# Kernel optimization log

Hardware: AMD Instinct MI355X
Metric: run time of the kernel (lower is better)

The kernel has to match this reference:

```python
import jax, jax.numpy as jnp
import numpy as np

IN_DIM = 256
OUT_DIM = 64   # per-head dim
NUM_HEADS = 8
B = 8
N = 1024


def setup_inputs() -> dict:
    key = jax.random.key(0)
    k_adj, k_h, kq, kk, kv, kbq, kbk, kbv = jax.random.split(key, 8)
    adj_matrix = jax.random.randint(k_adj, (N, N), 0, 2, dtype=jnp.int32)
    h = jax.random.normal(k_h, (B, N, IN_DIM), dtype=jnp.float32)
    s = 1.0 / np.sqrt(IN_DIM)
    Wq = jax.random.normal(kq, (IN_DIM, OUT_DIM * NUM_HEADS), dtype=jnp.float32) * s
    Wk = jax.random.normal(kk, (IN_DIM, OUT_DIM * NUM_HEADS), dtype=jnp.float32) * s
    Wv = jax.random.normal(kv, (IN_DIM, OUT_DIM * NUM_HEADS), dtype=jnp.float32) * s
    bq = jax.random.normal(kbq, (OUT_DIM * NUM_HEADS,), dtype=jnp.float32) * 0.01
    bk = jax.random.normal(kbk, (OUT_DIM * NUM_HEADS,), dtype=jnp.float32) * 0.01
    bv = jax.random.normal(kbv, (OUT_DIM * NUM_HEADS,), dtype=jnp.float32) * 0.01
    return {"adj_matrix": adj_matrix, "h": h, "Wq": Wq, "bq": bq,
            "Wk": Wk, "bk": bk, "Wv": Wv, "bv": bv}


def reference(adj_matrix, h, Wq, bq, Wk, bk, Wv, bv):
    B_, N_, _ = h.shape
    H, D = NUM_HEADS, OUT_DIM
    Qh = (h @ Wq + bq).reshape(B_, N_, H, D)
    Kh = (h @ Wk + bk).reshape(B_, N_, H, D)
    Vh = (h @ Wv + bv).reshape(B_, N_, H, D)
    scores = jnp.einsum('bnhd,bmhd->bhnm', Qh, Kh) / jnp.sqrt(jnp.float32(D))
    # adjacency mask broadcast over batch and heads (neigh_attention=True)
    scores = jnp.where(adj_matrix[None, None, :, :] == 0, -jnp.inf, scores)
    attn = jax.nn.softmax(scores, axis=-1)
    out = jnp.einsum('bhnm,bmhd->bnhd', attn, Vh)
    return out.reshape(B_, N_, H * D)
```

## Files before the change

### kernel.cpp

```cpp
#include <hip/hip_runtime.h>
#include <math.h>

#define IN_DIM 256
#define HD     512
#define NHEADS 8
#define DH     64
#define NSEQ   1024
#define BATCH  8

#define QSCALE 0.18033688011112042f

typedef unsigned short u16;
typedef unsigned int   u32;
typedef unsigned long long u64;
typedef short bf16x8 __attribute__((ext_vector_type(8)));
typedef float f32x4  __attribute__((ext_vector_type(4)));

#if __has_builtin(__builtin_amdgcn_exp2f)
#define EXP2(x) __builtin_amdgcn_exp2f(x)
#else
#define EXP2(x) __expf(0.69314718056f * (x))
#endif

static __device__ __forceinline__ u16 f2bf(float x) {
    u32 u = __builtin_bit_cast(u32, x);
    u += 0x7FFFu + ((u >> 16) & 1u);
    return (u16)(u >> 16);
}
static __device__ __forceinline__ float bf2f(u16 x) {
    return __builtin_bit_cast(float, ((u32)x) << 16);
}
static __device__ __forceinline__ u32 pk(u16 a, u16 b) {
    return (u32)a | ((u32)b << 16);
}
static __device__ __forceinline__ u32 cvtpk(float a, float b) {
    return pk(f2bf(a), f2bf(b));
}

__global__ __launch_bounds__(256)
void prep_kernel(const float* __restrict__ Wq, const float* __restrict__ Wk,
                 const float* __restrict__ Wv, const int* __restrict__ adj,
                 u16* __restrict__ Wt, u16* __restrict__ MaddT)
{
    __shared__ u32 shpool[64 * 65];
    const int bid = blockIdx.x, tid = threadIdx.x;

    if (bid < 96) {
        float* tile = (float*)shpool;
        const int wk = bid;
        const int k0 = (wk & 3) * 64, n0 = ((wk >> 2) & 7) * 64, wsel = wk >> 5;
        const float* W = (wsel == 0) ? Wq : (wsel == 1) ? Wk : Wv;
        u16* Out = Wt + (size_t)wsel * HD * IN_DIM;

        const int r = tid >> 2, c0 = (tid & 3) * 16;
#pragma unroll
        for (int j = 0; j < 16; j += 4) {
            float4 v = *(const float4*)(W + (size_t)(k0 + r) * HD + n0 + c0 + j);
            tile[r * 65 + c0 + j + 0] = v.x; tile[r * 65 + c0 + j + 1] = v.y;
            tile[r * 65 + c0 + j + 2] = v.z; tile[r * 65 + c0 + j + 3] = v.w;
        }
        __syncthreads();
        const int n = tid >> 2, ks = (tid & 3) * 16;
        u16 o[16];
#pragma unroll
        for (int j = 0; j < 16; ++j) o[j] = f2bf(tile[(ks + j) * 65 + n]);
        uint4 u0, u1;
        u0.x = pk(o[0], o[1]);   u0.y = pk(o[2], o[3]);
        u0.z = pk(o[4], o[5]);   u0.w = pk(o[6], o[7]);
        u1.x = pk(o[8], o[9]);   u1.y = pk(o[10], o[11]);
        u1.z = pk(o[12], o[13]); u1.w = pk(o[14], o[15]);
        u16* dst = Out + (size_t)(n0 + n) * IN_DIM + k0 + ks;
        *(uint4*)(dst) = u0;
        *(uint4*)(dst + 8) = u1;
    } else {
        int* tile = (int*)shpool;
        const int abid = bid - 96;
        const int tR = abid >> 4, tC = abid & 15;
        const int r = tid >> 2, cg = (tid & 3) * 16;
        const int* src = adj + (size_t)(tR * 64 + r) * NSEQ + tC * 64 + cg;
#pragma unroll
        for (int j = 0; j < 16; j += 4) {
            int4 a = *(const int4*)(src + j);
            tile[r * 65 + cg + j + 0] = a.x; tile[r * 65 + cg + j + 1] = a.y;
            tile[r * 65 + cg + j + 2] = a.z; tile[r * 65 + cg + j + 3] = a.w;
        }
        __syncthreads();
        const int kk = tid >> 2, qg = (tid & 3) * 16;
        u16 o[16];
#pragma unroll
        for (int j = 0; j < 16; ++j)
            o[j] = (tile[(qg + j) * 65 + kk] == 0) ? (u16)0xFF7F : (u16)0;
        uint4 u0, u1;
        u0.x = pk(o[0], o[1]);   u0.y = pk(o[2], o[3]);
        u0.z = pk(o[4], o[5]);   u0.w = pk(o[6], o[7]);
        u1.x = pk(o[8], o[9]);   u1.y = pk(o[10], o[11]);
        u1.z = pk(o[12], o[13]); u1.w = pk(o[14], o[15]);
        u16* dst = MaddT + (size_t)(tC * 64 + kk) * NSEQ + tR * 64 + qg;
        *(uint4*)(dst) = u0;
        *(uint4*)(dst + 8) = u1;
    }
}

__global__ __launch_bounds__(256, 2)
void qkv_gemm_kernel(const float* __restrict__ h, const u16* __restrict__ Wt,
                     const float* __restrict__ bq, const float* __restrict__ bk,
                     const float* __restrict__ bv,
                     u16* __restrict__ Qg, u16* __restrict__ Kg,
                     u16* __restrict__ Vtg)
{
    __shared__ u16 pool[128 * 64 + 3 * 64 * 64];
    u16* As = pool;
    u16* Bs = pool + 128 * 64;

    const int m0 = blockIdx.x * 128;
    const int hh = blockIdx.y;
    const int n0 = hh * 64;

    const int tid = threadIdx.x;
    const int w = tid >> 6, lane = tid & 63, l15 = lane & 15, quad = lane >> 4;
    const int sw = l15 & 7;

    f32x4 acc[3][2][4];
#pragma unroll
    for (int wh = 0; wh < 3; ++wh)
#pragma unroll
        for (int rs = 0; rs < 2; ++rs)
#pragma unroll
            for (int t = 0; t < 4; ++t) acc[wh][rs][t] = (f32x4){0.f, 0.f, 0.f, 0.f};

    const int arow = tid >> 1, acg = (tid & 1) * 4;
    const int brow = tid & 63, bgrp = tid >> 6;
    const float* srcA = h + (size_t)(m0 + arow) * IN_DIM;

    for (int kk = 0; kk < IN_DIM; kk += 64) {
        __syncthreads();
#pragma unroll
        for (int g = 0; g < 4; ++g) {
            const float* p = srcA + kk + (acg + g) * 8;
            float4 v0 = *(const float4*)(p);
            float4 v1 = *(const float4*)(p + 4);
            uint4 u;
            u.x = cvtpk(v0.x, v0.y); u.y = cvtpk(v0.z, v0.w);
            u.z = cvtpk(v1.x, v1.y); u.w = cvtpk(v1.z, v1.w);
            *(uint4*)&As[arow * 64 + (((acg + g) ^ (arow & 7)) * 8)] = u;
        }
#pragma unroll
        for (int i = 0; i < 6; ++i) {
            const int gc = bgrp * 6 + i;
            const int wh = gc >> 3, c8 = gc & 7;
            *(uint4*)&Bs[wh * 4096 + brow * 64 + ((c8 ^ (brow & 7)) * 8)] =
                *(const uint4*)(Wt + (size_t)wh * HD * IN_DIM +
                                (size_t)(n0 + brow) * IN_DIM + kk + c8 * 8);
        }
        __syncthreads();
        bf16x8 a[2][2];
#pragma unroll
        for (int rs = 0; rs < 2; ++rs) {
            const int ra = (w * 32 + rs * 16 + l15) * 64;
            a[rs][0] = *(const bf16x8*)&As[ra + ((quad ^ sw) * 8)];
            a[rs][1] = *(const bf16x8*)&As[ra + (((4 + quad) ^ sw) * 8)];
        }
#pragma unroll
        for (int t = 0; t < 4; ++t) {
            const int rb = (t * 16 + l15) * 64;
#pragma unroll
            for (int wh = 0; wh < 3; ++wh) {
                bf16x8 b0 = *(const bf16x8*)&Bs[wh * 4096 + rb + ((quad ^ sw) * 8)];
                bf16x8 b1 = *(const bf16x8*)&Bs[wh * 4096 + rb + (((4 + quad) ^ sw) * 8)];
#pragma unroll
                for (int rs = 0; rs < 2; ++rs) {
                    acc[wh][rs][t] = __builtin_amdgcn_mfma_f32_16x16x32_bf16(a[rs][0], b0, acc[wh][rs][t], 0, 0, 0);
                    acc[wh][rs][t] = __builtin_amdgcn_mfma_f32_16x16x32_bf16(a[rs][1], b1, acc[wh][rs][t], 0, 0, 0);
                }
            }
        }
    }

    for (int which = 0; which < 2; ++which) {
        u16* T = pool;
        const float* bias = (which == 0) ? bq : bk;
        u16* Out = (which == 0) ? Qg : Kg;
        const float scale = (which == 0) ? QSCALE : 1.0f;
        __syncthreads();
#pragma unroll
        for (int t = 0; t < 4; ++t) {
            const float bvv = bias[n0 + t * 16 + l15];
#pragma unroll
            for (int rs = 0; rs < 2; ++rs) {
                const int rowb = w * 32 + rs * 16 + quad * 4;
#pragma unroll
                for (int r = 0; r < 4; ++r)
                    T[(rowb + r) * 72 + t * 16 + l15] =
                        f2bf((acc[which][rs][t][r] + bvv) * scale);
            }
        }
        __syncthreads();
        const int row = tid >> 1, half = tid & 1;
        u16* dst = Out + (size_t)(m0 + row) * HD + n0 + half * 32;
        const u16* srcT = &T[row * 72 + half * 32];
#pragma unroll
        for (int i = 0; i < 4; ++i)
            *(uint4*)(dst + i * 8) = *(const uint4*)(srcT + i * 8);
    }

    {
        u16* T = pool;
        __syncthreads();
#pragma unroll
        for (int t = 0; t < 4; ++t) {
            const float bvv = bv[n0 + t * 16 + l15];
            const int trow = (t * 16 + l15) * 136;
#pragma unroll
            for (int rs = 0; rs < 2; ++rs) {
                const int base = w * 32 + rs * 16 + quad * 4;
                const int c64 = base >> 6;
                const int mloc = base & 63;
                const int cb = c64 * 64 + ((mloc & 15) * 4) + (mloc >> 4);
#pragma unroll
                for (int r = 0; r < 4; ++r)
                    T[trow + cb + 4 * r] = f2bf(acc[2][rs][t][r] + bvv);
            }
        }
        __syncthreads();
        const int b = m0 >> 10, nloc = m0 & 1023;
        const int d = tid >> 2, c = (tid & 3) * 32;
        u16* dst = Vtg + ((size_t)(b * NHEADS + hh) * DH + d) * NSEQ + nloc + c;
#pragma unroll
        for (int i = 0; i < 4; ++i)
            *(uint4*)(dst + i * 8) = *(uint4*)&T[d * 136 + c + i * 8];
    }
}

__global__ __launch_bounds__(512, 4)
void attn_kernel(const u16* __restrict__ MaddT, const u16* __restrict__ Qg,
                 const u16* __restrict__ Kg, const u16* __restrict__ Vtg,
                 float* __restrict__ out)
{
    __shared__ u16 Ks[2][64 * 64];
    __shared__ u16 Vs[2][64 * 64];
    __shared__ u16 Ps[128 * 64];

    const int tid = threadIdx.x;
    const int w = tid >> 6, lane = tid & 63, l15 = lane & 15, quad = lane >> 4;
    const int qt = blockIdx.x, bh = blockIdx.y;
    const int b = bh >> 3;
    const int n0 = qt * 128;
    const size_t rowbase = (size_t)b * NSEQ;
    const int colbase = (bh & 7) * DH;
    const int sw = l15 & 7;

    const u16* qrow = Qg + (rowbase + n0 + w * 16 + l15) * HD + colbase;
    const bf16x8 qa0 = *(const bf16x8*)(qrow + quad * 8);
    const bf16x8 qa1 = *(const bf16x8*)(qrow + 32 + quad * 8);

    const int srow = tid >> 3, c8w = tid & 7;
    const int swc = ((c8w ^ (srow & 7)) * 8);
    const u16* kgp = Kg + (rowbase + srow) * HD + colbase + c8w * 8;
    const u16* vgp = Vtg + ((size_t)bh * DH + srow) * NSEQ + c8w * 8;
    const u16* mgp = MaddT + (size_t)l15 * NSEQ + n0 + w * 16 + quad * 4;

    uint4 kG = *(const uint4*)kgp;
    uint4 vG = *(const uint4*)vgp;
    ushort4 mG[4];
#pragma unroll
    for (int t = 0; t < 4; ++t) mG[t] = *(const ushort4*)(mgp + (size_t)(t * 16) * NSEQ);

    *(uint4*)&Ks[0][srow * 64 + swc] = kG;
    *(uint4*)&Vs[0][srow * 64 + swc] = vG;
    __syncthreads();

    float lrow[4] = {0.f, 0.f, 0.f, 0.f};
    f32x4 O[4];
#pragma unroll
    for (int t = 0; t < 4; ++t) O[t] = (f32x4){0.f, 0.f, 0.f, 0.f};

    const int pwbase = (w * 16 + quad * 4) * 64;
    const int parow  = (w * 16 + l15) * 64;

    for (int ch = 0; ch < 16; ++ch) {
        const int cur = ch & 1;

        f32x4 s4[4];
#pragma unroll
        for (int t = 0; t < 4; ++t)
            s4[t] = (f32x4){bf2f(mG[t].x), bf2f(mG[t].y), bf2f(mG[t].z), bf2f(mG[t].w)};

        if (ch < 15) {
            kG = *(const uint4*)(kgp + (size_t)(ch + 1) * 64 * HD);
            vG = *(const uint4*)(vgp + (ch + 1) * 64);
#pragma unroll
            for (int t = 0; t < 4; ++t)
                mG[t] = *(const ushort4*)(mgp + ((size_t)(ch + 1) * 64 + t * 16) * NSEQ);
        }

#pragma unroll
        for (int t = 0; t < 4; ++t) {
            const int rb = (t * 16 + l15) * 64;
            bf16x8 kb0 = *(const bf16x8*)&Ks[cur][rb + ((quad ^ sw) * 8)];
            bf16x8 kb1 = *(const bf16x8*)&Ks[cur][rb + (((4 + quad) ^ sw) * 8)];
            s4[t] = __builtin_amdgcn_mfma_f32_16x16x32_bf16(qa0, kb0, s4[t], 0, 0, 0);
            s4[t] = __builtin_amdgcn_mfma_f32_16x16x32_bf16(qa1, kb1, s4[t], 0, 0, 0);
        }

        if (ch < 15) {
            *(uint4*)&Ks[1 - cur][srow * 64 + swc] = kG;
            *(uint4*)&Vs[1 - cur][srow * 64 + swc] = vG;
        }

#pragma unroll
        for (int r = 0; r < 4; ++r) {
            float p0 = EXP2(s4[0][r]);
            float p1 = EXP2(s4[1][r]);
            float p2 = EXP2(s4[2][r]);
            float p3 = EXP2(s4[3][r]);
            lrow[r] += (p0 + p1) + (p2 + p3);
            uint2 pw;
            pw.x = cvtpk(p0, p1);
            pw.y = cvtpk(p2, p3);
            const int q7 = (quad * 4 + r) & 7;
            *(uint2*)&Ps[pwbase + r * 64 + (((l15 >> 1) ^ q7) * 8) + (l15 & 1) * 4] = pw;
        }

        {
            bf16x8 pa0 = *(const bf16x8*)&Ps[parow + ((quad ^ sw) * 8)];
            bf16x8 pa1 = *(const bf16x8*)&Ps[parow + (((4 + quad) ^ sw) * 8)];
#pragma unroll
            for (int t = 0; t < 4; ++t) {
                const int rb = (t * 16 + l15) * 64;
                bf16x8 vb0 = *(const bf16x8*)&Vs[cur][rb + ((quad ^ sw) * 8)];
                bf16x8 vb1 = *(const bf16x8*)&Vs[cur][rb + (((4 + quad) ^ sw) * 8)];
                O[t] = __builtin_amdgcn_mfma_f32_16x16x32_bf16(pa0, vb0, O[t], 0, 0, 0);
                O[t] = __builtin_amdgcn_mfma_f32_16x16x32_bf16(pa1, vb1, O[t], 0, 0, 0);
            }
        }
        __syncthreads();
    }

#pragma unroll
    for (int d = 1; d < 16; d <<= 1)
#pragma unroll
        for (int r = 0; r < 4; ++r)
            lrow[r] += __shfl_xor(lrow[r], d, 64);

    float inv[4];
#pragma unroll
    for (int r = 0; r < 4; ++r) inv[r] = 1.0f / lrow[r];
#pragma unroll
    for (int t = 0; t < 4; ++t)
#pragma unroll
        for (int r = 0; r < 4; ++r)
            out[(rowbase + n0 + w * 16 + quad * 4 + r) * HD + colbase + t * 16 + l15] =
                O[t][r] * inv[r];
}

extern "C" void kernel_launch(void* const* d_in, const int* in_sizes, int n_in,
                              void* d_out, int out_size, void* d_ws, size_t ws_size,
                              hipStream_t stream) {
    const int*   adj = (const int*)d_in[0];
    const float* h   = (const float*)d_in[1];
    const float* Wq  = (const float*)d_in[2];
    const float* bq  = (const float*)d_in[3];
    const float* Wk  = (const float*)d_in[4];
    const float* bk  = (const float*)d_in[5];
    const float* Wv  = (const float*)d_in[6];
    const float* bv  = (const float*)d_in[7];
    float* outp = (float*)d_out;

    u16* Wt    = (u16*)d_ws;
    u16* Qg    = Wt + (size_t)3 * HD * IN_DIM;
    u16* Kg    = Qg + (size_t)BATCH * NSEQ * HD;
    u16* Vtg   = Kg + (size_t)BATCH * NSEQ * HD;
    u16* MaddT = Vtg + (size_t)BATCH * NSEQ * HD;

    prep_kernel<<<352, 256, 0, stream>>>(Wq, Wk, Wv, adj, Wt, MaddT);
    qkv_gemm_kernel<<<dim3(BATCH * NSEQ / 128, NHEADS), 256, 0, stream>>>(
        h, Wt, bq, bk, bv, Qg, Kg, Vtg);
    attn_kernel<<<dim3(NSEQ / 128, BATCH * NHEADS), 512, 0, stream>>>(
        MaddT, Qg, Kg, Vtg, outp);
}
```

Before: 142.8 us.

## Register-prefetch GEMM tiles and give each attention wave two row strips

The QKV GEMM now loads the next K-slice of h and W into registers while the current slice is computed, so global loads overlap the MFMAs. The attention kernel drops to 256 threads per block, and each wave handles 32 query rows instead of 16. This reuses every K/V LDS fragment across two MFMA row strips and halves the per-block cost of loading K and V tiles. The trade-off is higher register pressure and fewer waves to hide latency.

```diff
diff --git a/kernel.cpp b/kernel.cpp
--- a/kernel.cpp
+++ b/kernel.cpp
@@ -132,27 +132,50 @@
     const int brow = tid & 63, bgrp = tid >> 6;
     const float* srcA = h + (size_t)(m0 + arow) * IN_DIM;
 
+    float4 aF[8];
+    uint4  bF[6];
+#pragma unroll
+    for (int g = 0; g < 4; ++g) {
+        aF[2 * g]     = *(const float4*)(srcA + (acg + g) * 8);
+        aF[2 * g + 1] = *(const float4*)(srcA + (acg + g) * 8 + 4);
+    }
+#pragma unroll
+    for (int i = 0; i < 6; ++i) {
+        const int gc = bgrp * 6 + i, wh = gc >> 3, c8 = gc & 7;
+        bF[i] = *(const uint4*)(Wt + (size_t)wh * HD * IN_DIM +
+                                (size_t)(n0 + brow) * IN_DIM + c8 * 8);
+    }
+
     for (int kk = 0; kk < IN_DIM; kk += 64) {
         __syncthreads();
 #pragma unroll
         for (int g = 0; g < 4; ++g) {
-            const float* p = srcA + kk + (acg + g) * 8;
-            float4 v0 = *(const float4*)(p);
-            float4 v1 = *(const float4*)(p + 4);
             uint4 u;
-            u.x = cvtpk(v0.x, v0.y); u.y = cvtpk(v0.z, v0.w);
-            u.z = cvtpk(v1.x, v1.y); u.w = cvtpk(v1.z, v1.w);
+            u.x = cvtpk(aF[2 * g].x, aF[2 * g].y);
+            u.y = cvtpk(aF[2 * g].z, aF[2 * g].w);
+            u.z = cvtpk(aF[2 * g + 1].x, aF[2 * g + 1].y);
+            u.w = cvtpk(aF[2 * g + 1].z, aF[2 * g + 1].w);
             *(uint4*)&As[arow * 64 + (((acg + g) ^ (arow & 7)) * 8)] = u;
         }
 #pragma unroll
         for (int i = 0; i < 6; ++i) {
-            const int gc = bgrp * 6 + i;
-            const int wh = gc >> 3, c8 = gc & 7;
-            *(uint4*)&Bs[wh * 4096 + brow * 64 + ((c8 ^ (brow & 7)) * 8)] =
-                *(const uint4*)(Wt + (size_t)wh * HD * IN_DIM +
-                                (size_t)(n0 + brow) * IN_DIM + kk + c8 * 8);
-        }
-        __syncthreads();
+            const int gc = bgrp * 6 + i, wh = gc >> 3, c8 = gc & 7;
+            *(uint4*)&Bs[wh * 4096 + brow * 64 + ((c8 ^ (brow & 7)) * 8)] = bF[i];
+        }
+        __syncthreads();
+        if (kk + 64 < IN_DIM) {
+#pragma unroll
+            for (int g = 0; g < 4; ++g) {
+                aF[2 * g]     = *(const float4*)(srcA + kk + 64 + (acg + g) * 8);
+                aF[2 * g + 1] = *(const float4*)(srcA + kk + 64 + (acg + g) * 8 + 4);
+            }
+#pragma unroll
+            for (int i = 0; i < 6; ++i) {
+                const int gc = bgrp * 6 + i, wh = gc >> 3, c8 = gc & 7;
+                bF[i] = *(const uint4*)(Wt + (size_t)wh * HD * IN_DIM +
+                                        (size_t)(n0 + brow) * IN_DIM + kk + 64 + c8 * 8);
+            }
+        }
         bf16x8 a[2][2];
 #pragma unroll
         for (int rs = 0; rs < 2; ++rs) {
@@ -231,7 +254,7 @@
     }
 }
 
-__global__ __launch_bounds__(512, 4)
+__global__ __launch_bounds__(256, 3)
 void attn_kernel(const u16* __restrict__ MaddT, const u16* __restrict__ Qg,
                  const u16* __restrict__ Kg, const u16* __restrict__ Vtg,
                  float* __restrict__ out)
@@ -249,48 +272,63 @@
     const int colbase = (bh & 7) * DH;
     const int sw = l15 & 7;
 
-    const u16* qrow = Qg + (rowbase + n0 + w * 16 + l15) * HD + colbase;
-    const bf16x8 qa0 = *(const bf16x8*)(qrow + quad * 8);
-    const bf16x8 qa1 = *(const bf16x8*)(qrow + 32 + quad * 8);
-
-    const int srow = tid >> 3, c8w = tid & 7;
-    const int swc = ((c8w ^ (srow & 7)) * 8);
-    const u16* kgp = Kg + (rowbase + srow) * HD + colbase + c8w * 8;
-    const u16* vgp = Vtg + ((size_t)bh * DH + srow) * NSEQ + c8w * 8;
-    const u16* mgp = MaddT + (size_t)l15 * NSEQ + n0 + w * 16 + quad * 4;
-
-    uint4 kG = *(const uint4*)kgp;
-    uint4 vG = *(const uint4*)vgp;
-    ushort4 mG[4];
-#pragma unroll
-    for (int t = 0; t < 4; ++t) mG[t] = *(const ushort4*)(mgp + (size_t)(t * 16) * NSEQ);
-
-    *(uint4*)&Ks[0][srow * 64 + swc] = kG;
-    *(uint4*)&Vs[0][srow * 64 + swc] = vG;
+    bf16x8 qa[2][2];
+#pragma unroll
+    for (int rs = 0; rs < 2; ++rs) {
+        const u16* qrow = Qg + (rowbase + n0 + w * 32 + rs * 16 + l15) * HD + colbase;
+        qa[rs][0] = *(const bf16x8*)(qrow + quad * 8);
+        qa[rs][1] = *(const bf16x8*)(qrow + 32 + quad * 8);
+    }
+
+    const int srow = tid >> 2, cp = (tid & 3) * 2;
+    const int swc0 = ((cp ^ (srow & 7)) * 8), swc1 = (((cp + 1) ^ (srow & 7)) * 8);
+    const u16* kgp = Kg + (rowbase + srow) * HD + colbase + cp * 8;
+    const u16* vgp = Vtg + ((size_t)bh * DH + srow) * NSEQ + cp * 8;
+    const u16* mgp = MaddT + (size_t)l15 * NSEQ + n0 + w * 32 + quad * 4;
+
+    uint4 kG0 = *(const uint4*)kgp, kG1 = *(const uint4*)(kgp + 8);
+    uint4 vG0 = *(const uint4*)vgp, vG1 = *(const uint4*)(vgp + 8);
+    ushort4 mG[2][4];
+#pragma unroll
+    for (int rs = 0; rs < 2; ++rs)
+#pragma unroll
+        for (int t = 0; t < 4; ++t)
+            mG[rs][t] = *(const ushort4*)(mgp + (size_t)(t * 16) * NSEQ + rs * 16);
+
+    *(uint4*)&Ks[0][srow * 64 + swc0] = kG0;
+    *(uint4*)&Ks[0][srow * 64 + swc1] = kG1;
+    *(uint4*)&Vs[0][srow * 64 + swc0] = vG0;
+    *(uint4*)&Vs[0][srow * 64 + swc1] = vG1;
     __syncthreads();
 
-    float lrow[4] = {0.f, 0.f, 0.f, 0.f};
-    f32x4 O[4];
-#pragma unroll
-    for (int t = 0; t < 4; ++t) O[t] = (f32x4){0.f, 0.f, 0.f, 0.f};
-
-    const int pwbase = (w * 16 + quad * 4) * 64;
-    const int parow  = (w * 16 + l15) * 64;
+    float lrow[2][4] = {{0.f, 0.f, 0.f, 0.f}, {0.f, 0.f, 0.f, 0.f}};
+    f32x4 O[2][4];
+#pragma unroll
+    for (int rs = 0; rs < 2; ++rs)
+#pragma unroll
+        for (int t = 0; t < 4; ++t) O[rs][t] = (f32x4){0.f, 0.f, 0.f, 0.f};
 
     for (int ch = 0; ch < 16; ++ch) {
         const int cur = ch & 1;
 
-        f32x4 s4[4];
-#pragma unroll
-        for (int t = 0; t < 4; ++t)
-            s4[t] = (f32x4){bf2f(mG[t].x), bf2f(mG[t].y), bf2f(mG[t].z), bf2f(mG[t].w)};
+        f32x4 s4[2][4];
+#pragma unroll
+        for (int rs = 0; rs < 2; ++rs)
+#pragma unroll
+            for (int t = 0; t < 4; ++t)
+                s4[rs][t] = (f32x4){bf2f(mG[rs][t].x), bf2f(mG[rs][t].y),
+                                    bf2f(mG[rs][t].z), bf2f(mG[rs][t].w)};
 
         if (ch < 15) {
-            kG = *(const uint4*)(kgp + (size_t)(ch + 1) * 64 * HD);
-            vG = *(const uint4*)(vgp + (ch + 1) * 64);
-#pragma unroll
-            for (int t = 0; t < 4; ++t)
-                mG[t] = *(const ushort4*)(mgp + ((size_t)(ch + 1) * 64 + t * 16) * NSEQ);
+            kG0 = *(const uint4*)(kgp + (size_t)(ch + 1) * 64 * HD);
+            kG1 = *(const uint4*)(kgp + (size_t)(ch + 1) * 64 * HD + 8);
+            vG0 = *(const uint4*)(vgp + (ch + 1) * 64);
+            vG1 = *(const uint4*)(vgp + (ch + 1) * 64 + 8);
+#pragma unroll
+            for (int rs = 0; rs < 2; ++rs)
+#pragma unroll
+                for (int t = 0; t < 4; ++t)
+                    mG[rs][t] = *(const ushort4*)(mgp + ((size_t)(ch + 1) * 64 + t * 16) * NSEQ + rs * 16);
         }
 
 #pragma unroll
@@ -298,39 +336,55 @@
             const int rb = (t * 16 + l15) * 64;
             bf16x8 kb0 = *(const bf16x8*)&Ks[cur][rb + ((quad ^ sw) * 8)];
             bf16x8 kb1 = *(const bf16x8*)&Ks[cur][rb + (((4 + quad) ^ sw) * 8)];
-            s4[t] = __builtin_amdgcn_mfma_f32_16x16x32_bf16(qa0, kb0, s4[t], 0, 0, 0);
-            s4[t] = __builtin_amdgcn_mfma_f32_16x16x32_bf16(qa1, kb1, s4[t], 0, 0, 0);
+#pragma unroll
+            for (int rs = 0; rs < 2; ++rs) {
+                s4[rs][t] = __builtin_amdgcn_mfma_f32_16x16x32_bf16(qa[rs][0], kb0, s4[rs][t], 0, 0, 0);
+                s4[rs][t] = __builtin_amdgcn_mfma_f32_16x16x32_bf16(qa[rs][1], kb1, s4[rs][t], 0, 0, 0);
+            }
         }
 
         if (ch < 15) {
-            *(uint4*)&Ks[1 - cur][srow * 64 + swc] = kG;
-            *(uint4*)&Vs[1 - cur][srow * 64 + swc] = vG;
-        }
-
-#pragma unroll
-        for (int r = 0; r < 4; ++r) {
-            float p0 = EXP2(s4[0][r]);
-            float p1 = EXP2(s4[1][r]);
-            float p2 = EXP2(s4[2][r]);
-            float p3 = EXP2(s4[3][r]);
-            lrow[r] += (p0 + p1) + (p2 + p3);
-            uint2 pw;
-            pw.x = cvtpk(p0, p1);
-            pw.y = cvtpk(p2, p3);
-            const int q7 = (quad * 4 + r) & 7;
-            *(uint2*)&Ps[pwbase + r * 64 + (((l15 >> 1) ^ q7) * 8) + (l15 & 1) * 4] = pw;
-        }
+            *(uint4*)&Ks[1 - cur][srow * 64 + swc0] = kG0;
+            *(uint4*)&Ks[1 - cur][srow * 64 + swc1] = kG1;
+            *(uint4*)&Vs[1 - cur][srow * 64 + swc0] = vG0;
+            *(uint4*)&Vs[1 - cur][srow * 64 + swc1] = vG1;
+        }
+
+#pragma unroll
+        for (int rs = 0; rs < 2; ++rs)
+#pragma unroll
+            for (int r = 0; r < 4; ++r) {
+                float p0 = EXP2(s4[rs][0][r]);
+                float p1 = EXP2(s4[rs][1][r]);
+                float p2 = EXP2(s4[rs][2][r]);
+                float p3 = EXP2(s4[rs][3][r]);
+                lrow[rs][r] += (p0 + p1) + (p2 + p3);
+                uint2 pw;
+                pw.x = cvtpk(p0, p1);
+                pw.y = cvtpk(p2, p3);
+                const int q7 = (quad * 4 + r) & 7;
+                *(uint2*)&Ps[(w * 32 + rs * 16 + quad * 4 + r) * 64 +
+                             (((l15 >> 1) ^ q7) * 8) + (l15 & 1) * 4] = pw;
+            }
 
         {
-            bf16x8 pa0 = *(const bf16x8*)&Ps[parow + ((quad ^ sw) * 8)];
-            bf16x8 pa1 = *(const bf16x8*)&Ps[parow + (((4 + quad) ^ sw) * 8)];
+            bf16x8 pa[2][2];
+#pragma unroll
+            for (int rs = 0; rs < 2; ++rs) {
+                const int par = (w * 32 + rs * 16 + l15) * 64;
+                pa[rs][0] = *(const bf16x8*)&Ps[par + ((quad ^ sw) * 8)];
+                pa[rs][1] = *(const bf16x8*)&Ps[par + (((4 + quad) ^ sw) * 8)];
+            }
 #pragma unroll
             for (int t = 0; t < 4; ++t) {
                 const int rb = (t * 16 + l15) * 64;
                 bf16x8 vb0 = *(const bf16x8*)&Vs[cur][rb + ((quad ^ sw) * 8)];
                 bf16x8 vb1 = *(const bf16x8*)&Vs[cur][rb + (((4 + quad) ^ sw) * 8)];
-                O[t] = __builtin_amdgcn_mfma_f32_16x16x32_bf16(pa0, vb0, O[t], 0, 0, 0);
-                O[t] = __builtin_amdgcn_mfma_f32_16x16x32_bf16(pa1, vb1, O[t], 0, 0, 0);
+#pragma unroll
+                for (int rs = 0; rs < 2; ++rs) {
+                    O[rs][t] = __builtin_amdgcn_mfma_f32_16x16x32_bf16(pa[rs][0], vb0, O[rs][t], 0, 0, 0);
+                    O[rs][t] = __builtin_amdgcn_mfma_f32_16x16x32_bf16(pa[rs][1], vb1, O[rs][t], 0, 0, 0);
+                }
             }
         }
         __syncthreads();
@@ -339,18 +393,23 @@
 #pragma unroll
     for (int d = 1; d < 16; d <<= 1)
 #pragma unroll
-        for (int r = 0; r < 4; ++r)
-            lrow[r] += __shfl_xor(lrow[r], d, 64);
-
-    float inv[4];
-#pragma unroll
-    for (int r = 0; r < 4; ++r) inv[r] = 1.0f / lrow[r];
-#pragma unroll
-    for (int t = 0; t < 4; ++t)
-#pragma unroll
-        for (int r = 0; r < 4; ++r)
-            out[(rowbase + n0 + w * 16 + quad * 4 + r) * HD + colbase + t * 16 + l15] =
-                O[t][r] * inv[r];
+        for (int rs = 0; rs < 2; ++rs)
+#pragma unroll
+            for (int r = 0; r < 4; ++r)
+                lrow[rs][r] += __shfl_xor(lrow[rs][r], d, 64);
+
+#pragma unroll
+    for (int rs = 0; rs < 2; ++rs) {
+        float inv[4];
+#pragma unroll
+        for (int r = 0; r < 4; ++r) inv[r] = 1.0f / lrow[rs][r];
+#pragma unroll
+        for (int t = 0; t < 4; ++t)
+#pragma unroll
+            for (int r = 0; r < 4; ++r)
+                out[(rowbase + n0 + w * 32 + rs * 16 + quad * 4 + r) * HD +
+                    colbase + t * 16 + l15] = O[rs][t][r] * inv[r];
+    }
 }
 
 extern "C" void kernel_launch(void* const* d_in, const int* in_sizes, int n_in,
@@ -375,6 +434,6 @@
     prep_kernel<<<352, 256, 0, stream>>>(Wq, Wk, Wv, adj, Wt, MaddT);
     qkv_gemm_kernel<<<dim3(BATCH * NSEQ / 128, NHEADS), 256, 0, stream>>>(
         h, Wt, bq, bk, bv, Qg, Kg, Vtg);
-    attn_kernel<<<dim3(NSEQ / 128, BATCH * NHEADS), 512, 0, stream>>>(
+    attn_kernel<<<dim3(NSEQ / 128, BATCH * NHEADS), 256, 0, stream>>>(
         MaddT, Qg, Kg, Vtg, outp);
 }
```

Measured after the change: 158.7 us. +11.2%, slower.
